# Optimization experiments

Measured on AMD Instinct MI355X. Metric: run time of the kernel, lower is better.

## Reference

```python
import jax, jax.numpy as jnp
import numpy as np

NUM_TOPICS = 100
VOCAB = 8192
MC_N = 20
MD_N = 20
LAMBDA_D = 0.7
LAMBDA_A = 100.0
WARMUP_RATIO = 0.5
NUM_EPOCHS = 200


def setup_inputs() -> dict:
    key = jax.random.key(0)
    k1, k2 = jax.random.split(key)
    beta = jax.random.normal(k1, (NUM_TOPICS, VOCAB), dtype=jnp.float32)
    W = jax.random.uniform(k2, (VOCAB, VOCAB), dtype=jnp.float32)
    # fill_diagonal_(1) in __init__
    d = jnp.arange(VOCAB)
    W = W.at[d, d].set(1.0)
    return {"beta": beta, "coherence_weight": W, "epoch": 120}


def reference(beta, coherence_weight, epoch):
    K, V = beta.shape
    rows = jnp.arange(K)[:, None]

    # --- Mc: top-Mc_n mask -> additive -99999 on non-topk entries ---
    _, mc_idx = jax.lax.top_k(beta, MC_N)                      # [K, Mc_n]
    Mc = jnp.zeros_like(beta).at[rows, mc_idx].set(1.0)        # [K, V]
    Mc_add = (1.0 - Mc) * (-99999.0)

    # softmax over masked beta is detached in the original
    p = jax.lax.stop_gradient(jax.nn.softmax(beta + Mc_add, axis=1))
    M = p @ coherence_weight                                    # [K, V]

    # row-wise min-max normalize, then Wc = 1 - normalized
    m_min = jnp.min(M, axis=1, keepdims=True)
    m_max = jnp.max(M, axis=1, keepdims=True)
    Wc = 1.0 - (M - m_min) / (m_max - m_min)

    loss = 100.0 * jax.nn.softmax(beta, axis=1) ** 2 * Wc       # [K, V]

    # --- diversity mask Md (lambda_d > 0.5 branch) ---
    _, md_idx = jax.lax.top_k(beta, MD_N)
    Md_mask = jnp.zeros_like(beta).at[rows, md_idx].set(1.0)    # [K, V]
    # Md[t, v] = any other row has v in its top-Md_n
    col_sum = jnp.sum(Md_mask, axis=0)                          # [V]
    Md = (col_sum[None, :] - Md_mask) > 0                       # [K, V] bool

    pos = jnp.sum(jnp.where(Md, loss, 0.0))
    neg = jnp.sum(jnp.where(Md, 0.0, loss))
    total = (pos * LAMBDA_D + neg * (1.0 - LAMBDA_D)) * 2.0

    warmup_epochs = int(WARMUP_RATIO * NUM_EPOCHS)              # 100
    lambda_a_delta = LAMBDA_A / warmup_epochs
    lambda_a = epoch * lambda_a_delta if epoch < warmup_epochs else LAMBDA_A
    return lambda_a * total
```

## Files before the change

### kernel.cpp

```cpp
#include <hip/hip_runtime.h>
#include <math.h>

#define NT 100
#define VOCAB 8192
#define TOPN 20
#define CAP 4096

__global__ __launch_bounds__(1024) void topk_kernel(
    const float* __restrict__ beta,
    int*   __restrict__ top_idx,
    float* __restrict__ top_p,
    float* __restrict__ rowstats,
    float* __restrict__ out)
{
    const int k = blockIdx.x;
    const int t = threadIdx.x;
    if (k == 0 && t == 0) *out = 0.f;

    __shared__ float sred[16];
    __shared__ int   sredi[16];
    __shared__ int   s_base;
    __shared__ float cu[CAP];
    __shared__ unsigned short ci[CAP];
    __shared__ float s_winv[TOPN];
    __shared__ int   s_wini[TOPN];
    __shared__ float s_ps;

    const float* row = beta + (size_t)k * VOCAB;

    float4 r0 = *reinterpret_cast<const float4*>(row + (size_t)t * 4);
    float4 r1 = *reinterpret_cast<const float4*>(row + (size_t)(1024 + t) * 4);

    float mx = fmaxf(fmaxf(fmaxf(r0.x, r0.y), fmaxf(r0.z, r0.w)),
                     fmaxf(fmaxf(r1.x, r1.y), fmaxf(r1.z, r1.w)));
#pragma unroll
    for (int off = 32; off >= 1; off >>= 1) mx = fmaxf(mx, __shfl_down(mx, off));
    if ((t & 63) == 0) sred[t >> 6] = mx;
    __syncthreads();
    float rowmax = sred[0];
#pragma unroll
    for (int w = 1; w < 16; ++w) rowmax = fmaxf(rowmax, sred[w]);
    __syncthreads();

    float T = rowmax - 2.0f;
    for (int guard = 0; guard < 64; ++guard) {
        int c = 0;
        c += (r0.x >= T) + (r0.y >= T) + (r0.z >= T) + (r0.w >= T);
        c += (r1.x >= T) + (r1.y >= T) + (r1.z >= T) + (r1.w >= T);
#pragma unroll
        for (int off = 32; off >= 1; off >>= 1) c += __shfl_down(c, off);
        if ((t & 63) == 0) sredi[t >> 6] = c;
        __syncthreads();
        int cnt = 0;
#pragma unroll
        for (int w = 0; w < 16; ++w) cnt += sredi[w];
        if (cnt >= TOPN) break;
        T -= 0.5f;
        __syncthreads();
    }
    if (t == 0) s_base = 0;
    __syncthreads();

#pragma unroll
    for (int i = 0; i < 2; ++i) {
        const float4 rr = (i == 0) ? r0 : r1;
#pragma unroll
        for (int e = 0; e < 4; ++e) {
            const float v = (&rr.x)[e];
            const int idx = (i * 1024 + t) * 4 + e;
            const bool pr = (v >= T);
            const unsigned long long mask = __ballot(pr);
            const int lane = t & 63;
            const int pre = __popcll(mask & ((1ull << lane) - 1ull));
            int base = 0;
            if (lane == 0) base = atomicAdd(&s_base, __popcll(mask));
            base = __shfl(base, 0);
            if (pr) {
                const int p = base + pre;
                if (p < CAP) { cu[p] = v; ci[p] = (unsigned short)idx; }
            }
        }
    }
    __syncthreads();
    const int ncand = min(s_base, CAP);

    if (t < 64) {
        for (int it = 0; it < TOPN; ++it) {
            float bv = -INFINITY; int bp = -1;
            for (int p = t; p < ncand; p += 64) {
                const float v = cu[p];
                if (v > bv) { bv = v; bp = p; }
            }
#pragma unroll
            for (int off = 32; off >= 1; off >>= 1) {
                const float ov = __shfl_down(bv, off);
                const int   op = __shfl_down(bp, off);
                if (ov > bv) { bv = ov; bp = op; }
            }
            bp = __shfl(bp, 0);
            bv = __shfl(bv, 0);
            if (t == 0) { s_winv[it] = bv; s_wini[it] = ci[bp]; }
            cu[bp] = -INFINITY;
        }
    }
    __syncthreads();

    if (t == 0) {
        float ps = 0.f;
#pragma unroll
        for (int j = 0; j < TOPN; ++j) ps += expf(s_winv[j] - rowmax);
        s_ps = ps;
    }
    __syncthreads();
    if (t < TOPN) {
        top_idx[k * TOPN + t] = s_wini[t];
        top_p[k * TOPN + t]   = expf(s_winv[t] - rowmax) / s_ps;
    }

    float se = expf(r0.x - rowmax) + expf(r0.y - rowmax)
             + expf(r0.z - rowmax) + expf(r0.w - rowmax)
             + expf(r1.x - rowmax) + expf(r1.y - rowmax)
             + expf(r1.z - rowmax) + expf(r1.w - rowmax);
#pragma unroll
    for (int off = 32; off >= 1; off >>= 1) se += __shfl_down(se, off);
    if ((t & 63) == 0) sred[t >> 6] = se;
    __syncthreads();
    if (t == 0) {
        float s = 0.f;
#pragma unroll
        for (int w = 0; w < 16; ++w) s += sred[w];
        rowstats[2 * k + 0] = rowmax;
        rowstats[2 * k + 1] = s;
    }
}

__global__ __launch_bounds__(512) void fused_kernel(
    const float* __restrict__ beta,
    const float* __restrict__ W,
    const int*   __restrict__ top_idx,
    const float* __restrict__ top_p,
    const float* __restrict__ rowstats,
    const int*   __restrict__ epoch,
    float* __restrict__ out)
{
    const int k = blockIdx.x;
    const int t = threadIdx.x;

    __shared__ int   cnt[VOCAB];
    __shared__ int   sIdx[TOPN];
    __shared__ float sP[TOPN];
    __shared__ float sA[8], sB[8], sC[8], sD[8], sE[8], sF[8];

    if (t < TOPN) { sIdx[t] = top_idx[k * TOPN + t]; sP[t] = top_p[k * TOPN + t]; }
#pragma unroll
    for (int i = 0; i < VOCAB / 512; ++i) cnt[i * 512 + t] = 0;
    __syncthreads();

#pragma unroll 4
    for (int e = t; e < NT * TOPN; e += 512) atomicAdd(&cnt[top_idx[e]], 1);
    if (t < TOPN) atomicSub(&cnt[sIdx[t]], 1);

    int   idx_r[TOPN];
    float p_r[TOPN];
#pragma unroll
    for (int j = 0; j < TOPN; ++j) { idx_r[j] = sIdx[j]; p_r[j] = sP[j]; }

    const float rmax = rowstats[2 * k + 0];
    const float rinv = 1.0f / rowstats[2 * k + 1];

    __syncthreads();

    float mn = INFINITY, mxv = -INFINITY;
    float Apos = 0.f, Bpos = 0.f, Aneg = 0.f, Bneg = 0.f;

#pragma unroll
    for (int s = 0; s < 4; ++s) {
        const int col = s * 2048 + t * 4;

        float4 m = make_float4(0.f, 0.f, 0.f, 0.f);
#pragma unroll
        for (int j = 0; j < TOPN; ++j) {
            const float4 w = *reinterpret_cast<const float4*>(W + (size_t)idx_r[j] * VOCAB + col);
            const float pj = p_r[j];
            m.x += pj * w.x; m.y += pj * w.y; m.z += pj * w.z; m.w += pj * w.w;
        }
        mn  = fminf(mn,  fminf(fminf(m.x, m.y), fminf(m.z, m.w)));
        mxv = fmaxf(mxv, fmaxf(fmaxf(m.x, m.y), fmaxf(m.z, m.w)));

        const float4 bv = *reinterpret_cast<const float4*>(beta + (size_t)k * VOCAB + col);
        float4 w4;
        w4.x = expf(bv.x - rmax) * rinv;  w4.x = 100.f * w4.x * w4.x;
        w4.y = expf(bv.y - rmax) * rinv;  w4.y = 100.f * w4.y * w4.y;
        w4.z = expf(bv.z - rmax) * rinv;  w4.z = 100.f * w4.z * w4.z;
        w4.w = expf(bv.w - rmax) * rinv;  w4.w = 100.f * w4.w * w4.w;

        const int4 c4 = *reinterpret_cast<const int4*>(cnt + col);
        if (c4.x > 0) { Apos += w4.x; Bpos += w4.x * m.x; } else { Aneg += w4.x; Bneg += w4.x * m.x; }
        if (c4.y > 0) { Apos += w4.y; Bpos += w4.y * m.y; } else { Aneg += w4.y; Bneg += w4.y * m.y; }
        if (c4.z > 0) { Apos += w4.z; Bpos += w4.z * m.z; } else { Aneg += w4.z; Bneg += w4.z * m.z; }
        if (c4.w > 0) { Apos += w4.w; Bpos += w4.w * m.w; } else { Aneg += w4.w; Bneg += w4.w * m.w; }
    }

#pragma unroll
    for (int off = 32; off >= 1; off >>= 1) {
        mn   = fminf(mn,  __shfl_down(mn,  off));
        mxv  = fmaxf(mxv, __shfl_down(mxv, off));
        Apos += __shfl_down(Apos, off);
        Bpos += __shfl_down(Bpos, off);
        Aneg += __shfl_down(Aneg, off);
        Bneg += __shfl_down(Bneg, off);
    }
    if ((t & 63) == 0) {
        const int w = t >> 6;
        sA[w] = mn; sB[w] = mxv; sC[w] = Apos; sD[w] = Bpos; sE[w] = Aneg; sF[w] = Bneg;
    }
    __syncthreads();
    if (t == 0) {
        float a = sA[0], b = sB[0], Ap = 0.f, Bp = 0.f, An = 0.f, Bn = 0.f;
#pragma unroll
        for (int w = 0; w < 8; ++w) {
            a  = fminf(a, sA[w]);
            b  = fmaxf(b, sB[w]);
            Ap += sC[w]; Bp += sD[w]; An += sE[w]; Bn += sF[w];
        }
        const float inv = 1.0f / (b - a);
        const float pos = Ap - inv * (Bp - a * Ap);
        const float neg = An - inv * (Bn - a * An);
        const int e = *epoch;
        const float la = (e < 100) ? (float)e : 100.0f;
        atomicAdd(out, la * (pos * 0.7f + neg * 0.3f) * 2.0f);
    }
}

extern "C" void kernel_launch(void* const* d_in, const int* in_sizes, int n_in,
                              void* d_out, int out_size, void* d_ws, size_t ws_size,
                              hipStream_t stream)
{
    (void)in_sizes; (void)n_in; (void)out_size; (void)ws_size;
    const float* beta  = (const float*)d_in[0];
    const float* W     = (const float*)d_in[1];
    const int*   epoch = (const int*)d_in[2];
    float* out = (float*)d_out;

    char* ws = (char*)d_ws;
    int*   top_idx  = (int*)ws;    ws += NT * TOPN * sizeof(int);
    float* top_p    = (float*)ws;  ws += NT * TOPN * sizeof(float);
    float* rowstats = (float*)ws;  ws += NT * 2 * sizeof(float);

    topk_kernel<<<NT, 1024, 0, stream>>>(beta, top_idx, top_p, rowstats, out);
    fused_kernel<<<NT, 512, 0, stream>>>(beta, W, top_idx, top_p, rowstats, epoch, out);
}
```

Baseline: 53.55 us.

## Fuse W gather into top-k kernel and split diversity sum into sparse pass

The top-k kernel now also gathers the 20 W rows, builds M, writes it to workspace, and computes full-row sums A and B together with the min and max of M. This removes the separate fused kernel's re-read of beta and its per-block histogram of all top indices. A second kernel with 20 blocks of 5 topics each rebuilds the column-count histogram once per block and adds only the diversity-masked positives, rewriting the total as 0.6*all + 0.8*pos. The cost is a 3.2 MB round trip of M through global memory and a much smaller second grid.

After: 80.13 us. +49.6%, slower.

```diff
diff --git a/kernel.cpp b/kernel.cpp
--- a/kernel.cpp
+++ b/kernel.cpp
@@ -5,12 +5,15 @@
 #define VOCAB 8192
 #define TOPN 20
 #define CAP 4096
-
-__global__ __launch_bounds__(1024) void topk_kernel(
+#define N2B 20
+#define TPB 5
+
+__global__ __launch_bounds__(1024) void topk_gather_kernel(
     const float* __restrict__ beta,
+    const float* __restrict__ W,
     int*   __restrict__ top_idx,
-    float* __restrict__ top_p,
-    float* __restrict__ rowstats,
+    float* __restrict__ M,
+    float* __restrict__ stats,
     float* __restrict__ out)
 {
     const int k = blockIdx.x;
@@ -25,9 +28,12 @@
     __shared__ float s_winv[TOPN];
     __shared__ int   s_wini[TOPN];
     __shared__ float s_ps;
+    __shared__ float s_rsum;
+    __shared__ int   sIdx[TOPN];
+    __shared__ float sP[TOPN];
+    __shared__ float sA[16], sB[16], sC[16], sD[16];
 
     const float* row = beta + (size_t)k * VOCAB;
-
     float4 r0 = *reinterpret_cast<const float4*>(row + (size_t)t * 4);
     float4 r1 = *reinterpret_cast<const float4*>(row + (size_t)(1024 + t) * 4);
 
@@ -112,10 +118,6 @@
         s_ps = ps;
     }
     __syncthreads();
-    if (t < TOPN) {
-        top_idx[k * TOPN + t] = s_wini[t];
-        top_p[k * TOPN + t]   = expf(s_winv[t] - rowmax) / s_ps;
-    }
 
     float se = expf(r0.x - rowmax) + expf(r0.y - rowmax)
              + expf(r0.z - rowmax) + expf(r0.w - rowmax)
@@ -129,54 +131,27 @@
         float s = 0.f;
 #pragma unroll
         for (int w = 0; w < 16; ++w) s += sred[w];
-        rowstats[2 * k + 0] = rowmax;
-        rowstats[2 * k + 1] = s;
-    }
-}
-
-__global__ __launch_bounds__(512) void fused_kernel(
-    const float* __restrict__ beta,
-    const float* __restrict__ W,
-    const int*   __restrict__ top_idx,
-    const float* __restrict__ top_p,
-    const float* __restrict__ rowstats,
-    const int*   __restrict__ epoch,
-    float* __restrict__ out)
-{
-    const int k = blockIdx.x;
-    const int t = threadIdx.x;
-
-    __shared__ int   cnt[VOCAB];
-    __shared__ int   sIdx[TOPN];
-    __shared__ float sP[TOPN];
-    __shared__ float sA[8], sB[8], sC[8], sD[8], sE[8], sF[8];
-
-    if (t < TOPN) { sIdx[t] = top_idx[k * TOPN + t]; sP[t] = top_p[k * TOPN + t]; }
-#pragma unroll
-    for (int i = 0; i < VOCAB / 512; ++i) cnt[i * 512 + t] = 0;
-    __syncthreads();
-
-#pragma unroll 4
-    for (int e = t; e < NT * TOPN; e += 512) atomicAdd(&cnt[top_idx[e]], 1);
-    if (t < TOPN) atomicSub(&cnt[sIdx[t]], 1);
+        s_rsum = s;
+    }
+    if (t < TOPN) {
+        sIdx[t] = s_wini[t];
+        sP[t]   = expf(s_winv[t] - rowmax) / s_ps;
+        top_idx[k * TOPN + t] = s_wini[t];
+    }
+    __syncthreads();
+
+    const float rsum = s_rsum;
+    const float rinv = 1.0f / rsum;
 
     int   idx_r[TOPN];
     float p_r[TOPN];
 #pragma unroll
     for (int j = 0; j < TOPN; ++j) { idx_r[j] = sIdx[j]; p_r[j] = sP[j]; }
 
-    const float rmax = rowstats[2 * k + 0];
-    const float rinv = 1.0f / rowstats[2 * k + 1];
-
-    __syncthreads();
-
-    float mn = INFINITY, mxv = -INFINITY;
-    float Apos = 0.f, Bpos = 0.f, Aneg = 0.f, Bneg = 0.f;
-
-#pragma unroll
-    for (int s = 0; s < 4; ++s) {
-        const int col = s * 2048 + t * 4;
-
+    float mn = INFINITY, mxv = -INFINITY, Asum = 0.f, Bsum = 0.f;
+#pragma unroll
+    for (int seg = 0; seg < 2; ++seg) {
+        const int col = seg * 4096 + t * 4;
         float4 m = make_float4(0.f, 0.f, 0.f, 0.f);
 #pragma unroll
         for (int j = 0; j < TOPN; ++j) {
@@ -184,51 +159,114 @@
             const float pj = p_r[j];
             m.x += pj * w.x; m.y += pj * w.y; m.z += pj * w.z; m.w += pj * w.w;
         }
+        *reinterpret_cast<float4*>(M + (size_t)k * VOCAB + col) = m;
         mn  = fminf(mn,  fminf(fminf(m.x, m.y), fminf(m.z, m.w)));
         mxv = fmaxf(mxv, fmaxf(fmaxf(m.x, m.y), fmaxf(m.z, m.w)));
 
-        const float4 bv = *reinterpret_cast<const float4*>(beta + (size_t)k * VOCAB + col);
+        const float4 bb = (seg == 0) ? r0 : r1;
         float4 w4;
-        w4.x = expf(bv.x - rmax) * rinv;  w4.x = 100.f * w4.x * w4.x;
-        w4.y = expf(bv.y - rmax) * rinv;  w4.y = 100.f * w4.y * w4.y;
-        w4.z = expf(bv.z - rmax) * rinv;  w4.z = 100.f * w4.z * w4.z;
-        w4.w = expf(bv.w - rmax) * rinv;  w4.w = 100.f * w4.w * w4.w;
-
-        const int4 c4 = *reinterpret_cast<const int4*>(cnt + col);
-        if (c4.x > 0) { Apos += w4.x; Bpos += w4.x * m.x; } else { Aneg += w4.x; Bneg += w4.x * m.x; }
-        if (c4.y > 0) { Apos += w4.y; Bpos += w4.y * m.y; } else { Aneg += w4.y; Bneg += w4.y * m.y; }
-        if (c4.z > 0) { Apos += w4.z; Bpos += w4.z * m.z; } else { Aneg += w4.z; Bneg += w4.z * m.z; }
-        if (c4.w > 0) { Apos += w4.w; Bpos += w4.w * m.w; } else { Aneg += w4.w; Bneg += w4.w * m.w; }
+        w4.x = expf(bb.x - rowmax) * rinv;  w4.x = 100.f * w4.x * w4.x;
+        w4.y = expf(bb.y - rowmax) * rinv;  w4.y = 100.f * w4.y * w4.y;
+        w4.z = expf(bb.z - rowmax) * rinv;  w4.z = 100.f * w4.z * w4.z;
+        w4.w = expf(bb.w - rowmax) * rinv;  w4.w = 100.f * w4.w * w4.w;
+        Asum += w4.x + w4.y + w4.z + w4.w;
+        Bsum += w4.x * m.x + w4.y * m.y + w4.z * m.z + w4.w * m.w;
     }
 
 #pragma unroll
     for (int off = 32; off >= 1; off >>= 1) {
         mn   = fminf(mn,  __shfl_down(mn,  off));
         mxv  = fmaxf(mxv, __shfl_down(mxv, off));
-        Apos += __shfl_down(Apos, off);
-        Bpos += __shfl_down(Bpos, off);
-        Aneg += __shfl_down(Aneg, off);
-        Bneg += __shfl_down(Bneg, off);
+        Asum += __shfl_down(Asum, off);
+        Bsum += __shfl_down(Bsum, off);
     }
     if ((t & 63) == 0) {
         const int w = t >> 6;
-        sA[w] = mn; sB[w] = mxv; sC[w] = Apos; sD[w] = Bpos; sE[w] = Aneg; sF[w] = Bneg;
-    }
-    __syncthreads();
-    if (t == 0) {
-        float a = sA[0], b = sB[0], Ap = 0.f, Bp = 0.f, An = 0.f, Bn = 0.f;
-#pragma unroll
-        for (int w = 0; w < 8; ++w) {
-            a  = fminf(a, sA[w]);
-            b  = fmaxf(b, sB[w]);
-            Ap += sC[w]; Bp += sD[w]; An += sE[w]; Bn += sF[w];
-        }
-        const float inv = 1.0f / (b - a);
-        const float pos = Ap - inv * (Bp - a * Ap);
-        const float neg = An - inv * (Bn - a * An);
+        sA[w] = mn; sB[w] = mxv; sC[w] = Asum; sD[w] = Bsum;
+    }
+    __syncthreads();
+    if (t == 0) {
+        float a = sA[0], b = sB[0], A = 0.f, B = 0.f;
+#pragma unroll
+        for (int w = 0; w < 16; ++w) {
+            a = fminf(a, sA[w]); b = fmaxf(b, sB[w]);
+            A += sC[w]; B += sD[w];
+        }
+        float* s8 = stats + k * 8;
+        s8[0] = a; s8[1] = b; s8[2] = A; s8[3] = B; s8[4] = rowmax; s8[5] = rsum;
+    }
+}
+
+__global__ __launch_bounds__(512) void mdsum_kernel(
+    const float* __restrict__ beta,
+    const float* __restrict__ M,
+    const int*   __restrict__ top_idx,
+    const float* __restrict__ stats,
+    const int*   __restrict__ epoch,
+    float* __restrict__ out)
+{
+    const int b = blockIdx.x;
+    const int t = threadIdx.x;
+
+    __shared__ int cnt[VOCAB];
+    __shared__ unsigned own[VOCAB / 32];
+    __shared__ float sred[8];
+    __shared__ float s_block;
+
+    if (t == 0) s_block = 0.f;
+#pragma unroll
+    for (int i = 0; i < VOCAB / 512; ++i) cnt[i * 512 + t] = 0;
+    __syncthreads();
+    for (int e = t; e < NT * TOPN; e += 512) atomicAdd(&cnt[top_idx[e]], 1);
+    __syncthreads();
+
+    for (int kk = 0; kk < TPB; ++kk) {
+        const int k = b * TPB + kk;
+        if (t < VOCAB / 32) own[t] = 0u;
+        __syncthreads();
+        if (t < TOPN) {
+            const int v = top_idx[k * TOPN + t];
+            atomicOr(&own[v >> 5], 1u << (v & 31));
+        }
+        __syncthreads();
+
+        const float* s8 = stats + k * 8;
+        const float mn   = s8[0];
+        const float inv  = 1.0f / (s8[1] - mn);
+        const float rmax = s8[4];
+        const float rinv = 1.0f / s8[5];
+
+        float pos = 0.f;
+#pragma unroll
+        for (int seg = 0; seg < VOCAB / 512; ++seg) {
+            const int v = seg * 512 + t;
+            const int ob = (own[v >> 5] >> (v & 31)) & 1;
+            if (cnt[v] - ob > 0) {
+                const float mv = M[(size_t)k * VOCAB + v];
+                float w4 = expf(beta[(size_t)k * VOCAB + v] - rmax) * rinv;
+                w4 = 100.f * w4 * w4;
+                pos += w4 * (1.0f - (mv - mn) * inv);
+            }
+        }
+#pragma unroll
+        for (int off = 32; off >= 1; off >>= 1) pos += __shfl_down(pos, off);
+        if ((t & 63) == 0) sred[t >> 6] = pos;
+        __syncthreads();
+        if (t == 0) {
+            float p = 0.f;
+#pragma unroll
+            for (int w = 0; w < 8; ++w) p += sred[w];
+            const float A = s8[2], B = s8[3];
+            const float sum_all = A - inv * (B - mn * A);
+            s_block += 0.6f * sum_all + 0.8f * p;
+        }
+        __syncthreads();
+    }
+
+    if (t == 0) {
         const int e = *epoch;
         const float la = (e < 100) ? (float)e : 100.0f;
-        atomicAdd(out, la * (pos * 0.7f + neg * 0.3f) * 2.0f);
+        atomicAdd(out, la * s_block);
     }
 }
 
@@ -243,10 +281,11 @@
     float* out = (float*)d_out;
 
     char* ws = (char*)d_ws;
-    int*   top_idx  = (int*)ws;    ws += NT * TOPN * sizeof(int);
-    float* top_p    = (float*)ws;  ws += NT * TOPN * sizeof(float);
-    float* rowstats = (float*)ws;  ws += NT * 2 * sizeof(float);
-
-    topk_kernel<<<NT, 1024, 0, stream>>>(beta, top_idx, top_p, rowstats, out);
-    fused_kernel<<<NT, 512, 0, stream>>>(beta, W, top_idx, top_p, rowstats, epoch, out);
+    int*   top_idx = (int*)ws;    ws += NT * TOPN * sizeof(int);
+    float* stats   = (float*)ws;  ws += NT * 8 * sizeof(float);
+    ws = (char*)(((size_t)ws + 255) & ~(size_t)255);
+    float* M       = (float*)ws;  ws += (size_t)NT * VOCAB * sizeof(float);
+
+    topk_gather_kernel<<<NT, 1024, 0, stream>>>(beta, W, top_idx, M, stats, out);
+    mdsum_kernel<<<N2B, 512, 0, stream>>>(beta, M, top_idx, stats, epoch, out);
 }
```
